# Optimization experiments

Measured on AMD Instinct MI355X. Metric: run time of the kernel, lower is better.

Reference implementation:

```python
import jax, jax.numpy as jnp
import numpy as np

B, C, H, W = 4, 192, 56, 56


def setup_inputs() -> dict:
    key = jax.random.key(0)
    k1, k2, k3 = jax.random.split(key, 3)
    x = jax.random.normal(k1, (B, C, H, W), dtype=jnp.float32)
    conv_w = jax.random.normal(k2, (C, 2 * C), dtype=jnp.float32) * (1.0 / np.sqrt(2 * C))
    conv_b = jax.random.normal(k3, (C,), dtype=jnp.float32) * 0.01
    bn_gamma = jnp.ones((C,), dtype=jnp.float32)
    bn_beta = jnp.zeros((C,), dtype=jnp.float32)
    bn_mean = jnp.zeros((C,), dtype=jnp.float32)
    bn_var = jnp.ones((C,), dtype=jnp.float32)
    return {"x": x, "conv_w": conv_w, "conv_b": conv_b, "bn_gamma": bn_gamma,
            "bn_beta": bn_beta, "bn_mean": bn_mean, "bn_var": bn_var, "K": 4}


def reference(x, conv_w, conv_b, bn_gamma, bn_beta, bn_mean, bn_var, K):
    b, c, h, w = x.shape
    shifts_h = list(range(0, h, K))          # rolls along H
    shifts_w = list(range(K, w, K))          # rolls along W
    n = len(shifts_h) + len(shifts_w)
    scale = n ** (-0.5)
    # (B, n, C, H, W): all circularly shifted copies (static shift set)
    rolled = jnp.stack([jnp.roll(x, i, axis=2) for i in shifts_h] +
                       [jnp.roll(x, j, axis=3) for j in shifts_w], axis=1)
    # scores: tanh(scale * x * x_rolled), summed over channels -> (B, n, 1, H, W)
    scores = jnp.tanh(rolled * x[:, None] * scale).sum(axis=2, keepdims=True)
    weights = jax.nn.softmax(scores, axis=1)
    out = (rolled * weights).sum(axis=1)     # (B, C, H, W)
    cat = jnp.concatenate([x, out], axis=1)  # (B, 2C, H, W)
    # 1x1 conv as GEMM over channels
    y = jnp.einsum('bchw,oc->bohw', cat, conv_w) + conv_b[None, :, None, None]
    # BatchNorm2d in eval mode (running stats)
    eps = 1e-5
    inv = bn_gamma / jnp.sqrt(bn_var + eps)
    y = (y - bn_mean[None, :, None, None]) * inv[None, :, None, None] + bn_beta[None, :, None, None]
    return jax.nn.gelu(y, approximate=False)
```

## Files before the change

kernel.cpp:

```cpp
#include <hip/hip_runtime.h>
#include <hip/hip_bf16.h>
#include <math.h>

#define BB 4
#define CC 192
#define HH 56
#define WW 56
#define HWW 3136

typedef __attribute__((ext_vector_type(8))) short short8;
typedef __attribute__((ext_vector_type(4))) float f32x4;

__device__ __forceinline__ unsigned short f2b(float f) {
    __hip_bfloat16 h = __float2bfloat16(f);
    return __builtin_bit_cast(unsigned short, h);
}
__device__ __forceinline__ float b2f(unsigned short u) {
    unsigned int x = ((unsigned int)u) << 16;
    return __builtin_bit_cast(float, x);
}
__device__ __forceinline__ void fma4(float4& a, float w, const float4& x) {
    a.x += w * x.x; a.y += w * x.y; a.z += w * x.z; a.w += w * x.w;
}

__global__ __launch_bounds__(256) void k_pre(const float* __restrict__ x,
                                             float* __restrict__ xt,
                                             const float* __restrict__ cw,
                                             unsigned short* __restrict__ cwh,
                                             unsigned short* __restrict__ cwl) {
    int tid = threadIdx.x;
    if (blockIdx.x < 2352) {
        __shared__ float tile[32][33];
        int id = blockIdx.x;
        int b = id / 588, rem = id % 588;
        int by = rem / 98, bx = rem % 98;
        int tx = tid & 31, ty = tid >> 5;
        int p0 = bx * 32, c0 = by * 32;
#pragma unroll
        for (int i = 0; i < 4; i++) {
            int c = c0 + ty + 8 * i;
            tile[ty + 8 * i][tx] = x[(b * CC + c) * HWW + p0 + tx];
        }
        __syncthreads();
#pragma unroll
        for (int i = 0; i < 4; i++) {
            int p = p0 + ty + 8 * i;
            xt[(size_t)(b * HWW + p) * CC + c0 + tx] = tile[tx][ty + 8 * i];
        }
    } else {
        int i = (blockIdx.x - 2352) * 256 + tid;
        if (i < CC * 576) {
            int o = i / 576, k = i % 576;
            int ks = (k >= 384) ? (k - 192) : k;
            float v = cw[o * 384 + ks];
            unsigned short hi = f2b(v);
            cwh[i] = hi;
            cwl[i] = f2b(v - b2f(hi));
        }
    }
}

__global__ __launch_bounds__(256) void k_scores(const float* __restrict__ xt,
                                                float* __restrict__ sp) {
    __shared__ float Xs[28 * 100];
    int bid = blockIdx.x, tid = threadIdx.x;
    bool isH = bid < 896;
    int lid = isH ? bid : bid - 896;
    int half = lid & 1;
    int rp = (lid >> 1) & 1;
    int cb = lid >> 2;
    int b = cb / 56, l0 = cb % 56;
    int r0 = rp * 2;

    const float* src = xt + (size_t)(b * HWW) * CC + half * 96;
    for (int idx = tid; idx < 28 * 24; idx += 256) {
        int t2 = idx / 24, cq = idx % 24;
        int pi = (r0 + t2 / 14) + 4 * (t2 % 14);
        int pix = isH ? (pi * WW + l0) : (l0 * WW + pi);
        float4 v = *(const float4*)(src + (size_t)pix * CC + cq * 4);
        *(float4*)&Xs[t2 * 100 + cq * 4] = v;
    }
    __syncthreads();

    const float K2 = 0.38490017945975050f;
    int perCls = isH ? 105 : 91;
    int nI = 2 * perCls;
    if (tid < nI) {
        int cls = tid / perCls, p = tid % perCls;
        int a, bb;
        if (isH) {
            a = (int)((sqrtf((float)(8 * p + 1)) - 1.0f) * 0.5f);
            bb = p - (a * (a + 1)) / 2;
        } else {
            int ap = (int)((sqrtf((float)(8 * p + 1)) - 1.0f) * 0.5f);
            bb = p - (ap * (ap + 1)) / 2;
            a = ap + 1;
        }
        const float* pA = &Xs[(cls * 14 + a) * 100];
        const float* pB = &Xs[(cls * 14 + bb) * 100];
        float s0 = 0.f, s1 = 0.f, s2 = 0.f, s3 = 0.f;
#pragma unroll
        for (int q = 0; q < 24; q++) {
            float4 av = *(const float4*)(pA + q * 4);
            float4 bv = *(const float4*)(pB + q * 4);
            s0 += __builtin_amdgcn_rcpf(__expf(av.x * bv.x * K2) + 1.0f);
            s1 += __builtin_amdgcn_rcpf(__expf(av.y * bv.y * K2) + 1.0f);
            s2 += __builtin_amdgcn_rcpf(__expf(av.z * bv.z * K2) + 1.0f);
            s3 += __builtin_amdgcn_rcpf(__expf(av.w * bv.w * K2) + 1.0f);
        }
        float s = 96.0f - 2.0f * (s0 + s1 + s2 + s3);
        int r = r0 + cls;
        size_t base = (size_t)(half * BB + b) * HWW;
        if (isH) {
            int i1 = a - bb;
            int h1 = r + 4 * a, h2 = r + 4 * bb;
            sp[(base + h1 * WW + l0) * 32 + i1] = s;
            if (a != bb) sp[(base + h2 * WW + l0) * 32 + (14 - i1)] = s;
        } else {
            int d = a - bb;
            int w1 = r + 4 * a, w2 = r + 4 * bb;
            sp[(base + l0 * WW + w1) * 32 + 14 + (d - 1)] = s;
            sp[(base + l0 * WW + w2) * 32 + 14 + (13 - d)] = s;
        }
    }
}

__global__ __launch_bounds__(192) void k_acc(const float* __restrict__ xt,
                                             const float* __restrict__ sp,
                                             unsigned short* __restrict__ oHh,
                                             unsigned short* __restrict__ oHl,
                                             unsigned short* __restrict__ oWh,
                                             unsigned short* __restrict__ oWl) {
    __shared__ float Wt[14 * 56];
    int bid = blockIdx.x, tid = threadIdx.x;
    bool isH = bid < 224;
    int lid = isH ? bid : bid - 224;
    int b = lid / 56, l0 = lid % 56;

    if (tid < 56) {
        int pix = isH ? (tid * WW + l0) : (l0 * WW + tid);
        const float4* p0 = (const float4*)&sp[((size_t)(0 * BB + b) * HWW + pix) * 32];
        const float4* p1 = (const float4*)&sp[((size_t)(1 * BB + b) * HWW + pix) * 32];
        float sc[28];
#pragma unroll
        for (int j = 0; j < 7; j++) {
            float4 u = p0[j], v = p1[j];
            sc[4 * j + 0] = u.x + v.x; sc[4 * j + 1] = u.y + v.y;
            sc[4 * j + 2] = u.z + v.z; sc[4 * j + 3] = u.w + v.w;
        }
        float mx = -1e30f;
#pragma unroll
        for (int s = 0; s < 27; s++) mx = fmaxf(mx, sc[s]);
        float sum = 0.f;
#pragma unroll
        for (int s = 0; s < 27; s++) { sc[s] = __expf(sc[s] - mx); sum += sc[s]; }
        float inv = __builtin_amdgcn_rcpf(sum);
        if (isH) {
#pragma unroll
            for (int i = 0; i < 14; i++) Wt[i * 56 + tid] = sc[i] * inv;
        } else {
#pragma unroll
            for (int j = 0; j < 13; j++) Wt[j * 56 + tid] = sc[14 + j] * inv;
        }
    }
    __syncthreads();
    {
        int r = tid & 3, q = tid >> 2;
        float4 in[14];
#pragma unroll
        for (int t = 0; t < 14; t++) {
            int pix = isH ? ((r + 4 * t) * WW + l0) : (l0 * WW + (r + 4 * t));
            in[t] = *(const float4*)(xt + (size_t)(b * HWW + pix) * CC + q * 4);
        }
        float4 acc[14] = {};
        if (isH) {
#pragma unroll
            for (int i = 0; i < 14; i++)
#pragma unroll
                for (int a = 0; a < 14; a++)
                    fma4(acc[a], Wt[i * 56 + (r + 4 * a)], in[(a - i + 14) % 14]);
        } else {
#pragma unroll
            for (int j = 0; j < 13; j++)
#pragma unroll
                for (int a = 0; a < 14; a++)
                    fma4(acc[a], Wt[j * 56 + (r + 4 * a)], in[(a - j - 1 + 14) % 14]);
        }
        unsigned short* dh = isH ? oHh : oWh;
        unsigned short* dl = isH ? oHl : oWl;
#pragma unroll
        for (int a = 0; a < 14; a++) {
            int pix = isH ? ((r + 4 * a) * WW + l0) : (l0 * WW + (r + 4 * a));
            size_t o = (size_t)(b * HWW + pix) * CC + q * 4;
            ushort4 hi4, lo4;
            hi4.x = f2b(acc[a].x); lo4.x = f2b(acc[a].x - b2f(hi4.x));
            hi4.y = f2b(acc[a].y); lo4.y = f2b(acc[a].y - b2f(hi4.y));
            hi4.z = f2b(acc[a].z); lo4.z = f2b(acc[a].z - b2f(hi4.z));
            hi4.w = f2b(acc[a].w); lo4.w = f2b(acc[a].w - b2f(hi4.w));
            *(ushort4*)(dh + o) = hi4;
            *(ushort4*)(dl + o) = lo4;
        }
    }
}

__global__ __launch_bounds__(256) void k_conv(const float* __restrict__ xt,
                                              const unsigned short* __restrict__ oHh,
                                              const unsigned short* __restrict__ oHl,
                                              const unsigned short* __restrict__ oWh,
                                              const unsigned short* __restrict__ oWl,
                                              const unsigned short* __restrict__ cwh,
                                              const unsigned short* __restrict__ cwl,
                                              const float* __restrict__ cb,
                                              const float* __restrict__ gma,
                                              const float* __restrict__ bta,
                                              const float* __restrict__ mea,
                                              const float* __restrict__ var,
                                              float* __restrict__ y) {
    __shared__ unsigned short AB[4 * 64 * 72];
    unsigned short* Ah = AB;
    unsigned short* Al = AB + 64 * 72;
    unsigned short* Bh = AB + 2 * 64 * 72;
    unsigned short* Bl = AB + 3 * 64 * 72;
    int bm = blockIdx.x * 64, bn = blockIdx.y * 64;
    int tid = threadIdx.x, lane = tid & 63, wv = tid >> 6;

    f32x4 acc[4] = {{0,0,0,0},{0,0,0,0},{0,0,0,0},{0,0,0,0}};

    for (int kc9 = 0; kc9 < 9; kc9++) {
#pragma unroll
        for (int r2 = 0; r2 < 2; r2++) {
            int idx = tid + r2 * 256;
            int m = idx >> 3, kq = idx & 7;
            if (kc9 < 3) {
                const float* s = xt + (size_t)(bm + m) * CC + kc9 * 64 + kq * 8;
                float4 v0 = *(const float4*)s;
                float4 v1 = *(const float4*)(s + 4);
                float v[8] = {v0.x, v0.y, v0.z, v0.w, v1.x, v1.y, v1.z, v1.w};
                unsigned short hi[8], lo[8];
#pragma unroll
                for (int e = 0; e < 8; e++) {
                    hi[e] = f2b(v[e]);
                    lo[e] = f2b(v[e] - b2f(hi[e]));
                }
                *(short8*)&Ah[m * 72 + kq * 8] = *(short8*)hi;
                *(short8*)&Al[m * 72 + kq * 8] = *(short8*)lo;
            } else {
                const unsigned short* sh;
                const unsigned short* sl;
                int coff;
                if (kc9 < 6) { sh = oHh; sl = oHl; coff = (kc9 - 3) * 64; }
                else         { sh = oWh; sl = oWl; coff = (kc9 - 6) * 64; }
                size_t ao = (size_t)(bm + m) * CC + coff + kq * 8;
                *(short8*)&Ah[m * 72 + kq * 8] = *(const short8*)(sh + ao);
                *(short8*)&Al[m * 72 + kq * 8] = *(const short8*)(sl + ao);
            }
            size_t bo = (size_t)(bn + m) * 576 + kc9 * 64 + kq * 8;
            *(short8*)&Bh[m * 72 + kq * 8] = *(const short8*)(cwh + bo);
            *(short8*)&Bl[m * 72 + kq * 8] = *(const short8*)(cwl + bo);
        }
        __syncthreads();
        int n0 = wv * 16;
        int k8 = lane >> 4;
        int col = lane & 15;
#pragma unroll
        for (int ks = 0; ks < 64; ks += 32) {
            int koff = ks + k8 * 8;
            short8 bfh = *(const short8*)&Bh[(n0 + col) * 72 + koff];
            short8 bfl = *(const short8*)&Bl[(n0 + col) * 72 + koff];
#pragma unroll
            for (int fm = 0; fm < 4; fm++) {
                short8 afh = *(const short8*)&Ah[(fm * 16 + col) * 72 + koff];
                short8 afl = *(const short8*)&Al[(fm * 16 + col) * 72 + koff];
                acc[fm] = __builtin_amdgcn_mfma_f32_16x16x32_bf16(afh, bfh, acc[fm], 0, 0, 0);
                acc[fm] = __builtin_amdgcn_mfma_f32_16x16x32_bf16(afl, bfh, acc[fm], 0, 0, 0);
                acc[fm] = __builtin_amdgcn_mfma_f32_16x16x32_bf16(afh, bfl, acc[fm], 0, 0, 0);
            }
        }
        __syncthreads();
    }

    float* Ds = (float*)AB;
    {
        int col = lane & 15, rowq = lane >> 4;
#pragma unroll
        for (int fm = 0; fm < 4; fm++)
#pragma unroll
            for (int rg = 0; rg < 4; rg++)
                Ds[(fm * 16 + rowq * 4 + rg) * 68 + wv * 16 + col] = acc[fm][rg];
    }
    __syncthreads();
    {
        int o = tid >> 2, mq0 = tid & 3;
        int oo = bn + o;
        float bias = cb[oo];
        float inv  = gma[oo] * rsqrtf(var[oo] + 1e-5f);
        float mean = mea[oo], beta = bta[oo];
        int b = bm / HWW, p0 = bm % HWW;
#pragma unroll
        for (int g = 0; g < 4; g++) {
            int mq = mq0 + g * 4;
            float v[4];
#pragma unroll
            for (int j = 0; j < 4; j++) {
                float t = Ds[(mq * 4 + j) * 68 + o] + bias;
                t = (t - mean) * inv + beta;
                v[j] = 0.5f * t * (1.0f + erff(t * 0.70710678118654752f));
            }
            float4 st; st.x = v[0]; st.y = v[1]; st.z = v[2]; st.w = v[3];
            *(float4*)&y[(size_t)(b * CC + oo) * HWW + p0 + mq * 4] = st;
        }
    }
}

extern "C" void kernel_launch(void* const* d_in, const int* in_sizes, int n_in,
                              void* d_out, int out_size, void* d_ws, size_t ws_size,
                              hipStream_t stream) {
    const float* x   = (const float*)d_in[0];
    const float* cw  = (const float*)d_in[1];
    const float* cb  = (const float*)d_in[2];
    const float* gma = (const float*)d_in[3];
    const float* bta = (const float*)d_in[4];
    const float* mea = (const float*)d_in[5];
    const float* var = (const float*)d_in[6];
    float* out = (float*)d_out;

    float* ws = (float*)d_ws;
    float*          xt  = ws;
    float*          sp  = ws + 2408448;
    unsigned short* oHh = (unsigned short*)(ws + 3211264);
    unsigned short* oHl = (unsigned short*)(ws + 4415488);
    unsigned short* oWh = (unsigned short*)(ws + 5619712);
    unsigned short* oWl = (unsigned short*)(ws + 6823936);
    unsigned short* cwh = (unsigned short*)(ws + 8028160);
    unsigned short* cwl = (unsigned short*)(ws + 8083456);

    k_pre<<<2784, 256, 0, stream>>>(x, xt, cw, cwh, cwl);
    k_scores<<<1792, 256, 0, stream>>>(xt, sp);
    k_acc<<<448, 192, 0, stream>>>(xt, sp, oHh, oHl, oWh, oWl);
    k_conv<<<dim3(196, 3), 256, 0, stream>>>(xt, oHh, oHl, oWh, oWl,
                                             cwh, cwl, cb, gma, bta, mea, var, out);
}
```

Measured before the change: 132.2 us.

## Apply 1x1 conv before shift-weighted accumulation and fuse epilogue into W pass

Uses linearity of the 1x1 conv to compute W·x once (N=384, K=192) before the softmax-weighted shifted sums, so the accumulation operates on projected features instead of feeding a K=576 GEMM. The scores computation and GEMM share one launch, and BN+GELU are fused into the W-direction accumulation kernel with an LDS transpose for NCHW output. It trades bf16 split intermediates for fp32 u/z/yp buffers and leaves the accumulation kernels with only 224 blocks each.

```diff
diff --git a/kernel.cpp b/kernel.cpp
--- a/kernel.cpp
+++ b/kernel.cpp
@@ -24,15 +24,14 @@
 }
 
 __global__ __launch_bounds__(256) void k_pre(const float* __restrict__ x,
+                                             const float* __restrict__ cw,
                                              float* __restrict__ xt,
-                                             const float* __restrict__ cw,
                                              unsigned short* __restrict__ cwh,
                                              unsigned short* __restrict__ cwl) {
-    int tid = threadIdx.x;
-    if (blockIdx.x < 2352) {
+    int tid = threadIdx.x, bid = blockIdx.x;
+    if (bid < 2352) {
         __shared__ float tile[32][33];
-        int id = blockIdx.x;
-        int b = id / 588, rem = id % 588;
+        int b = bid / 588, rem = bid % 588;
         int by = rem / 98, bx = rem % 98;
         int tx = tid & 31, ty = tid >> 5;
         int p0 = bx * 32, c0 = by * 32;
@@ -48,11 +47,10 @@
             xt[(size_t)(b * HWW + p) * CC + c0 + tx] = tile[tx][ty + 8 * i];
         }
     } else {
-        int i = (blockIdx.x - 2352) * 256 + tid;
-        if (i < CC * 576) {
-            int o = i / 576, k = i % 576;
-            int ks = (k >= 384) ? (k - 192) : k;
-            float v = cw[o * 384 + ks];
+        int i = (bid - 2352) * 256 + tid;
+        if (i < 384 * 192) {
+            int n = i / 192, k = i % 192;
+            float v = (n < 192) ? cw[n * 384 + k] : cw[(n - 192) * 384 + 192 + k];
             unsigned short hi = f2b(v);
             cwh[i] = hi;
             cwl[i] = f2b(v - b2f(hi));
@@ -60,93 +58,173 @@
     }
 }
 
-__global__ __launch_bounds__(256) void k_scores(const float* __restrict__ xt,
-                                                float* __restrict__ sp) {
-    __shared__ float Xs[28 * 100];
-    int bid = blockIdx.x, tid = threadIdx.x;
-    bool isH = bid < 896;
-    int lid = isH ? bid : bid - 896;
-    int half = lid & 1;
-    int rp = (lid >> 1) & 1;
-    int cb = lid >> 2;
-    int b = cb / 56, l0 = cb % 56;
-    int r0 = rp * 2;
-
-    const float* src = xt + (size_t)(b * HWW) * CC + half * 96;
-    for (int idx = tid; idx < 28 * 24; idx += 256) {
-        int t2 = idx / 24, cq = idx % 24;
-        int pi = (r0 + t2 / 14) + 4 * (t2 % 14);
-        int pix = isH ? (pi * WW + l0) : (l0 * WW + pi);
-        float4 v = *(const float4*)(src + (size_t)pix * CC + cq * 4);
-        *(float4*)&Xs[t2 * 100 + cq * 4] = v;
-    }
-    __syncthreads();
-
-    const float K2 = 0.38490017945975050f;
-    int perCls = isH ? 105 : 91;
-    int nI = 2 * perCls;
-    if (tid < nI) {
-        int cls = tid / perCls, p = tid % perCls;
-        int a, bb;
-        if (isH) {
-            a = (int)((sqrtf((float)(8 * p + 1)) - 1.0f) * 0.5f);
-            bb = p - (a * (a + 1)) / 2;
-        } else {
-            int ap = (int)((sqrtf((float)(8 * p + 1)) - 1.0f) * 0.5f);
-            bb = p - (ap * (ap + 1)) / 2;
-            a = ap + 1;
-        }
-        const float* pA = &Xs[(cls * 14 + a) * 100];
-        const float* pB = &Xs[(cls * 14 + bb) * 100];
-        float s0 = 0.f, s1 = 0.f, s2 = 0.f, s3 = 0.f;
-#pragma unroll
-        for (int q = 0; q < 24; q++) {
-            float4 av = *(const float4*)(pA + q * 4);
-            float4 bv = *(const float4*)(pB + q * 4);
-            s0 += __builtin_amdgcn_rcpf(__expf(av.x * bv.x * K2) + 1.0f);
-            s1 += __builtin_amdgcn_rcpf(__expf(av.y * bv.y * K2) + 1.0f);
-            s2 += __builtin_amdgcn_rcpf(__expf(av.z * bv.z * K2) + 1.0f);
-            s3 += __builtin_amdgcn_rcpf(__expf(av.w * bv.w * K2) + 1.0f);
-        }
-        float s = 96.0f - 2.0f * (s0 + s1 + s2 + s3);
-        int r = r0 + cls;
-        size_t base = (size_t)(half * BB + b) * HWW;
-        if (isH) {
-            int i1 = a - bb;
-            int h1 = r + 4 * a, h2 = r + 4 * bb;
-            sp[(base + h1 * WW + l0) * 32 + i1] = s;
-            if (a != bb) sp[(base + h2 * WW + l0) * 32 + (14 - i1)] = s;
-        } else {
-            int d = a - bb;
-            int w1 = r + 4 * a, w2 = r + 4 * bb;
-            sp[(base + l0 * WW + w1) * 32 + 14 + (d - 1)] = s;
-            sp[(base + l0 * WW + w2) * 32 + 14 + (13 - d)] = s;
-        }
-    }
-}
-
-__global__ __launch_bounds__(192) void k_acc(const float* __restrict__ xt,
-                                             const float* __restrict__ sp,
-                                             unsigned short* __restrict__ oHh,
-                                             unsigned short* __restrict__ oHl,
-                                             unsigned short* __restrict__ oWh,
-                                             unsigned short* __restrict__ oWl) {
+__global__ __launch_bounds__(256) void k_mid(const float* __restrict__ xt,
+                                             const unsigned short* __restrict__ cwh,
+                                             const unsigned short* __restrict__ cwl,
+                                             float* __restrict__ sp,
+                                             float* __restrict__ u,
+                                             float* __restrict__ z) {
+    __shared__ __align__(16) char smem[36864];
+    int tid = threadIdx.x, bid = blockIdx.x;
+
+    if (bid < 1792) {
+        float* Xs = (float*)smem;
+        const float K2 = 0.38490017945975050f;
+        bool isH = bid < 896;
+        int lid = isH ? bid : bid - 896;
+        int half = lid & 1;
+        int rp = (lid >> 1) & 1;
+        int cb2 = lid >> 2;
+        int b = cb2 / 56, l0 = cb2 % 56;
+        int r0 = rp * 2;
+
+        const float* src = xt + (size_t)(b * HWW) * CC + half * 96;
+        for (int idx = tid; idx < 28 * 24; idx += 256) {
+            int t2 = idx / 24, cq = idx % 24;
+            int pi = (r0 + t2 / 14) + 4 * (t2 % 14);
+            int pix = isH ? (pi * WW + l0) : (l0 * WW + pi);
+            float4 v = *(const float4*)(src + (size_t)pix * CC + cq * 4);
+            *(float4*)&Xs[t2 * 100 + cq * 4] = v;
+        }
+        __syncthreads();
+
+        int perCls = isH ? 105 : 91;
+        if (tid < 2 * perCls) {
+            int cls = tid / perCls, p = tid % perCls;
+            int a, bb;
+            if (isH) {
+                a = (int)((sqrtf((float)(8 * p + 1)) - 1.0f) * 0.5f);
+                bb = p - (a * (a + 1)) / 2;
+            } else {
+                int ap = (int)((sqrtf((float)(8 * p + 1)) - 1.0f) * 0.5f);
+                bb = p - (ap * (ap + 1)) / 2;
+                a = ap + 1;
+            }
+            const float* pA = &Xs[(cls * 14 + a) * 100];
+            const float* pB = &Xs[(cls * 14 + bb) * 100];
+            float s0 = 0.f, s1 = 0.f, s2 = 0.f, s3 = 0.f;
+#pragma unroll
+            for (int q = 0; q < 24; q++) {
+                float4 av = *(const float4*)(pA + q * 4);
+                float4 bv = *(const float4*)(pB + q * 4);
+                s0 += __builtin_amdgcn_rcpf(__expf(av.x * bv.x * K2) + 1.0f);
+                s1 += __builtin_amdgcn_rcpf(__expf(av.y * bv.y * K2) + 1.0f);
+                s2 += __builtin_amdgcn_rcpf(__expf(av.z * bv.z * K2) + 1.0f);
+                s3 += __builtin_amdgcn_rcpf(__expf(av.w * bv.w * K2) + 1.0f);
+            }
+            float s = 96.0f - 2.0f * (s0 + s1 + s2 + s3);
+            int r = r0 + cls;
+            size_t base = (size_t)(half * BB + b) * HWW;
+            if (isH) {
+                int i1 = a - bb;
+                int h1 = r + 4 * a, h2 = r + 4 * bb;
+                sp[(base + h1 * WW + l0) * 32 + i1] = s;
+                if (a != bb) sp[(base + h2 * WW + l0) * 32 + (14 - i1)] = s;
+            } else {
+                int d = a - bb;
+                int w1 = r + 4 * a, w2 = r + 4 * bb;
+                sp[(base + l0 * WW + w1) * 32 + 14 + (d - 1)] = s;
+                sp[(base + l0 * WW + w2) * 32 + 14 + (13 - d)] = s;
+            }
+        }
+        return;
+    }
+
+    {
+        unsigned short* Ah = (unsigned short*)smem;
+        unsigned short* Al = Ah + 64 * 72;
+        unsigned short* Bh = Ah + 2 * 64 * 72;
+        unsigned short* Bl = Ah + 3 * 64 * 72;
+        float* Ds = (float*)smem;
+        int vb = bid - 1792;
+        int bm = (vb % 196) * 64, bn = (vb / 196) * 64;
+        int lane = tid & 63, wv = tid >> 6;
+
+        f32x4 acc[4] = {{0,0,0,0},{0,0,0,0},{0,0,0,0},{0,0,0,0}};
+
+        for (int kc = 0; kc < 3; kc++) {
+#pragma unroll
+            for (int r2 = 0; r2 < 2; r2++) {
+                int idx = tid + r2 * 256;
+                int m = idx >> 3, kq = idx & 7;
+                const float* s = xt + (size_t)(bm + m) * CC + kc * 64 + kq * 8;
+                float4 v0 = *(const float4*)s;
+                float4 v1 = *(const float4*)(s + 4);
+                float vv[8] = {v0.x, v0.y, v0.z, v0.w, v1.x, v1.y, v1.z, v1.w};
+                unsigned short hi[8], lo[8];
+#pragma unroll
+                for (int e = 0; e < 8; e++) {
+                    hi[e] = f2b(vv[e]);
+                    lo[e] = f2b(vv[e] - b2f(hi[e]));
+                }
+                *(short8*)&Ah[m * 72 + kq * 8] = *(short8*)hi;
+                *(short8*)&Al[m * 72 + kq * 8] = *(short8*)lo;
+                size_t bo = (size_t)(bn + m) * 192 + kc * 64 + kq * 8;
+                *(short8*)&Bh[m * 72 + kq * 8] = *(const short8*)(cwh + bo);
+                *(short8*)&Bl[m * 72 + kq * 8] = *(const short8*)(cwl + bo);
+            }
+            __syncthreads();
+            int n0 = wv * 16;
+            int k8 = lane >> 4;
+            int col = lane & 15;
+#pragma unroll
+            for (int ks = 0; ks < 64; ks += 32) {
+                int koff = ks + k8 * 8;
+                short8 bfh = *(const short8*)&Bh[(n0 + col) * 72 + koff];
+                short8 bfl = *(const short8*)&Bl[(n0 + col) * 72 + koff];
+#pragma unroll
+                for (int fm = 0; fm < 4; fm++) {
+                    short8 afh = *(const short8*)&Ah[(fm * 16 + col) * 72 + koff];
+                    short8 afl = *(const short8*)&Al[(fm * 16 + col) * 72 + koff];
+                    acc[fm] = __builtin_amdgcn_mfma_f32_16x16x32_bf16(afh, bfh, acc[fm], 0, 0, 0);
+                    acc[fm] = __builtin_amdgcn_mfma_f32_16x16x32_bf16(afl, bfh, acc[fm], 0, 0, 0);
+                    acc[fm] = __builtin_amdgcn_mfma_f32_16x16x32_bf16(afh, bfl, acc[fm], 0, 0, 0);
+                }
+            }
+            __syncthreads();
+        }
+        {
+            int col = lane & 15, rowq = lane >> 4;
+#pragma unroll
+            for (int fm = 0; fm < 4; fm++)
+#pragma unroll
+                for (int rg = 0; rg < 4; rg++)
+                    Ds[(fm * 16 + rowq * 4 + rg) * 68 + wv * 16 + col] = acc[fm][rg];
+        }
+        __syncthreads();
+        {
+            int c4 = tid & 15, m0 = tid >> 4;
+            int cg = bn + c4 * 4;
+            float* dst = (cg < 192) ? u : z;
+            int cc = (cg < 192) ? cg : cg - 192;
+#pragma unroll
+            for (int p = 0; p < 4; p++) {
+                int m = m0 + p * 16;
+                float4 v = *(float4*)&Ds[m * 68 + c4 * 4];
+                *(float4*)&dst[(size_t)(bm + m) * CC + cc] = v;
+            }
+        }
+    }
+}
+
+__global__ __launch_bounds__(192) void k_accH(const float* __restrict__ u,
+                                              const float* __restrict__ z,
+                                              const float* __restrict__ sp,
+                                              float* __restrict__ yp) {
     __shared__ float Wt[14 * 56];
     int bid = blockIdx.x, tid = threadIdx.x;
-    bool isH = bid < 224;
-    int lid = isH ? bid : bid - 224;
-    int b = lid / 56, l0 = lid % 56;
+    int b = bid / 56, l0 = bid % 56;
 
     if (tid < 56) {
-        int pix = isH ? (tid * WW + l0) : (l0 * WW + tid);
+        int pix = tid * WW + l0;
         const float4* p0 = (const float4*)&sp[((size_t)(0 * BB + b) * HWW + pix) * 32];
         const float4* p1 = (const float4*)&sp[((size_t)(1 * BB + b) * HWW + pix) * 32];
         float sc[28];
 #pragma unroll
         for (int j = 0; j < 7; j++) {
-            float4 u = p0[j], v = p1[j];
-            sc[4 * j + 0] = u.x + v.x; sc[4 * j + 1] = u.y + v.y;
-            sc[4 * j + 2] = u.z + v.z; sc[4 * j + 3] = u.w + v.w;
+            float4 a = p0[j], v = p1[j];
+            sc[4 * j + 0] = a.x + v.x; sc[4 * j + 1] = a.y + v.y;
+            sc[4 * j + 2] = a.z + v.z; sc[4 * j + 3] = a.w + v.w;
         }
         float mx = -1e30f;
 #pragma unroll
@@ -155,13 +233,8 @@
 #pragma unroll
         for (int s = 0; s < 27; s++) { sc[s] = __expf(sc[s] - mx); sum += sc[s]; }
         float inv = __builtin_amdgcn_rcpf(sum);
-        if (isH) {
-#pragma unroll
-            for (int i = 0; i < 14; i++) Wt[i * 56 + tid] = sc[i] * inv;
-        } else {
-#pragma unroll
-            for (int j = 0; j < 13; j++) Wt[j * 56 + tid] = sc[14 + j] * inv;
-        }
+#pragma unroll
+        for (int i = 0; i < 14; i++) Wt[i * 56 + tid] = sc[i] * inv;
     }
     __syncthreads();
     {
@@ -169,145 +242,119 @@
         float4 in[14];
 #pragma unroll
         for (int t = 0; t < 14; t++) {
-            int pix = isH ? ((r + 4 * t) * WW + l0) : (l0 * WW + (r + 4 * t));
-            in[t] = *(const float4*)(xt + (size_t)(b * HWW + pix) * CC + q * 4);
-        }
-        float4 acc[14] = {};
-        if (isH) {
-#pragma unroll
-            for (int i = 0; i < 14; i++)
-#pragma unroll
-                for (int a = 0; a < 14; a++)
-                    fma4(acc[a], Wt[i * 56 + (r + 4 * a)], in[(a - i + 14) % 14]);
-        } else {
-#pragma unroll
-            for (int j = 0; j < 13; j++)
-#pragma unroll
-                for (int a = 0; a < 14; a++)
-                    fma4(acc[a], Wt[j * 56 + (r + 4 * a)], in[(a - j - 1 + 14) % 14]);
-        }
-        unsigned short* dh = isH ? oHh : oWh;
-        unsigned short* dl = isH ? oHl : oWl;
+            int pix = (r + 4 * t) * WW + l0;
+            in[t] = *(const float4*)(z + (size_t)(b * HWW + pix) * CC + q * 4);
+        }
+        float4 acc[14];
 #pragma unroll
         for (int a = 0; a < 14; a++) {
-            int pix = isH ? ((r + 4 * a) * WW + l0) : (l0 * WW + (r + 4 * a));
-            size_t o = (size_t)(b * HWW + pix) * CC + q * 4;
-            ushort4 hi4, lo4;
-            hi4.x = f2b(acc[a].x); lo4.x = f2b(acc[a].x - b2f(hi4.x));
-            hi4.y = f2b(acc[a].y); lo4.y = f2b(acc[a].y - b2f(hi4.y));
-            hi4.z = f2b(acc[a].z); lo4.z = f2b(acc[a].z - b2f(hi4.z));
-            hi4.w = f2b(acc[a].w); lo4.w = f2b(acc[a].w - b2f(hi4.w));
-            *(ushort4*)(dh + o) = hi4;
-            *(ushort4*)(dl + o) = lo4;
-        }
-    }
-}
-
-__global__ __launch_bounds__(256) void k_conv(const float* __restrict__ xt,
-                                              const unsigned short* __restrict__ oHh,
-                                              const unsigned short* __restrict__ oHl,
-                                              const unsigned short* __restrict__ oWh,
-                                              const unsigned short* __restrict__ oWl,
-                                              const unsigned short* __restrict__ cwh,
-                                              const unsigned short* __restrict__ cwl,
+            int pix = (r + 4 * a) * WW + l0;
+            acc[a] = *(const float4*)(u + (size_t)(b * HWW + pix) * CC + q * 4);
+        }
+#pragma unroll
+        for (int i = 0; i < 14; i++)
+#pragma unroll
+            for (int a = 0; a < 14; a++)
+                fma4(acc[a], Wt[i * 56 + (r + 4 * a)], in[(a - i + 14) % 14]);
+#pragma unroll
+        for (int a = 0; a < 14; a++) {
+            int pix = (r + 4 * a) * WW + l0;
+            *(float4*)(yp + (size_t)(b * HWW + pix) * CC + q * 4) = acc[a];
+        }
+    }
+}
+
+__global__ __launch_bounds__(192) void k_accW(const float* __restrict__ yp,
+                                              const float* __restrict__ z,
+                                              const float* __restrict__ sp,
                                               const float* __restrict__ cb,
                                               const float* __restrict__ gma,
                                               const float* __restrict__ bta,
                                               const float* __restrict__ mea,
                                               const float* __restrict__ var,
                                               float* __restrict__ y) {
-    __shared__ unsigned short AB[4 * 64 * 72];
-    unsigned short* Ah = AB;
-    unsigned short* Al = AB + 64 * 72;
-    unsigned short* Bh = AB + 2 * 64 * 72;
-    unsigned short* Bl = AB + 3 * 64 * 72;
-    int bm = blockIdx.x * 64, bn = blockIdx.y * 64;
-    int tid = threadIdx.x, lane = tid & 63, wv = tid >> 6;
-
-    f32x4 acc[4] = {{0,0,0,0},{0,0,0,0},{0,0,0,0},{0,0,0,0}};
-
-    for (int kc9 = 0; kc9 < 9; kc9++) {
-#pragma unroll
-        for (int r2 = 0; r2 < 2; r2++) {
-            int idx = tid + r2 * 256;
-            int m = idx >> 3, kq = idx & 7;
-            if (kc9 < 3) {
-                const float* s = xt + (size_t)(bm + m) * CC + kc9 * 64 + kq * 8;
-                float4 v0 = *(const float4*)s;
-                float4 v1 = *(const float4*)(s + 4);
-                float v[8] = {v0.x, v0.y, v0.z, v0.w, v1.x, v1.y, v1.z, v1.w};
-                unsigned short hi[8], lo[8];
-#pragma unroll
-                for (int e = 0; e < 8; e++) {
-                    hi[e] = f2b(v[e]);
-                    lo[e] = f2b(v[e] - b2f(hi[e]));
-                }
-                *(short8*)&Ah[m * 72 + kq * 8] = *(short8*)hi;
-                *(short8*)&Al[m * 72 + kq * 8] = *(short8*)lo;
-            } else {
-                const unsigned short* sh;
-                const unsigned short* sl;
-                int coff;
-                if (kc9 < 6) { sh = oHh; sl = oHl; coff = (kc9 - 3) * 64; }
-                else         { sh = oWh; sl = oWl; coff = (kc9 - 6) * 64; }
-                size_t ao = (size_t)(bm + m) * CC + coff + kq * 8;
-                *(short8*)&Ah[m * 72 + kq * 8] = *(const short8*)(sh + ao);
-                *(short8*)&Al[m * 72 + kq * 8] = *(const short8*)(sl + ao);
-            }
-            size_t bo = (size_t)(bn + m) * 576 + kc9 * 64 + kq * 8;
-            *(short8*)&Bh[m * 72 + kq * 8] = *(const short8*)(cwh + bo);
-            *(short8*)&Bl[m * 72 + kq * 8] = *(const short8*)(cwl + bo);
-        }
-        __syncthreads();
-        int n0 = wv * 16;
-        int k8 = lane >> 4;
-        int col = lane & 15;
-#pragma unroll
-        for (int ks = 0; ks < 64; ks += 32) {
-            int koff = ks + k8 * 8;
-            short8 bfh = *(const short8*)&Bh[(n0 + col) * 72 + koff];
-            short8 bfl = *(const short8*)&Bl[(n0 + col) * 72 + koff];
-#pragma unroll
-            for (int fm = 0; fm < 4; fm++) {
-                short8 afh = *(const short8*)&Ah[(fm * 16 + col) * 72 + koff];
-                short8 afl = *(const short8*)&Al[(fm * 16 + col) * 72 + koff];
-                acc[fm] = __builtin_amdgcn_mfma_f32_16x16x32_bf16(afh, bfh, acc[fm], 0, 0, 0);
-                acc[fm] = __builtin_amdgcn_mfma_f32_16x16x32_bf16(afl, bfh, acc[fm], 0, 0, 0);
-                acc[fm] = __builtin_amdgcn_mfma_f32_16x16x32_bf16(afh, bfl, acc[fm], 0, 0, 0);
-            }
-        }
-        __syncthreads();
-    }
-
-    float* Ds = (float*)AB;
-    {
-        int col = lane & 15, rowq = lane >> 4;
-#pragma unroll
-        for (int fm = 0; fm < 4; fm++)
-#pragma unroll
-            for (int rg = 0; rg < 4; rg++)
-                Ds[(fm * 16 + rowq * 4 + rg) * 68 + wv * 16 + col] = acc[fm][rg];
+    __shared__ float Wt[14 * 56];
+    __shared__ float Ys[56 * 196];
+    int bid = blockIdx.x, tid = threadIdx.x;
+    int b = bid / 56, l0 = bid % 56;
+
+    if (tid < 56) {
+        int pix = l0 * WW + tid;
+        const float4* p0 = (const float4*)&sp[((size_t)(0 * BB + b) * HWW + pix) * 32];
+        const float4* p1 = (const float4*)&sp[((size_t)(1 * BB + b) * HWW + pix) * 32];
+        float sc[28];
+#pragma unroll
+        for (int j = 0; j < 7; j++) {
+            float4 a = p0[j], v = p1[j];
+            sc[4 * j + 0] = a.x + v.x; sc[4 * j + 1] = a.y + v.y;
+            sc[4 * j + 2] = a.z + v.z; sc[4 * j + 3] = a.w + v.w;
+        }
+        float mx = -1e30f;
+#pragma unroll
+        for (int s = 0; s < 27; s++) mx = fmaxf(mx, sc[s]);
+        float sum = 0.f;
+#pragma unroll
+        for (int s = 0; s < 27; s++) { sc[s] = __expf(sc[s] - mx); sum += sc[s]; }
+        float inv = __builtin_amdgcn_rcpf(sum);
+#pragma unroll
+        for (int j = 0; j < 13; j++) Wt[j * 56 + tid] = sc[14 + j] * inv;
     }
     __syncthreads();
     {
-        int o = tid >> 2, mq0 = tid & 3;
-        int oo = bn + o;
-        float bias = cb[oo];
-        float inv  = gma[oo] * rsqrtf(var[oo] + 1e-5f);
-        float mean = mea[oo], beta = bta[oo];
-        int b = bm / HWW, p0 = bm % HWW;
-#pragma unroll
-        for (int g = 0; g < 4; g++) {
-            int mq = mq0 + g * 4;
-            float v[4];
-#pragma unroll
-            for (int j = 0; j < 4; j++) {
-                float t = Ds[(mq * 4 + j) * 68 + o] + bias;
-                t = (t - mean) * inv + beta;
-                v[j] = 0.5f * t * (1.0f + erff(t * 0.70710678118654752f));
-            }
-            float4 st; st.x = v[0]; st.y = v[1]; st.z = v[2]; st.w = v[3];
-            *(float4*)&y[(size_t)(b * CC + oo) * HWW + p0 + mq * 4] = st;
+        int r = tid & 3, q = tid >> 2;
+        float4 in[14];
+#pragma unroll
+        for (int t = 0; t < 14; t++) {
+            int pix = l0 * WW + (r + 4 * t);
+            in[t] = *(const float4*)(z + (size_t)(b * HWW + pix) * CC + q * 4);
+        }
+        float4 acc[14];
+#pragma unroll
+        for (int a = 0; a < 14; a++) {
+            int pix = l0 * WW + (r + 4 * a);
+            acc[a] = *(const float4*)(yp + (size_t)(b * HWW + pix) * CC + q * 4);
+        }
+#pragma unroll
+        for (int j = 0; j < 13; j++)
+#pragma unroll
+            for (int a = 0; a < 14; a++)
+                fma4(acc[a], Wt[j * 56 + (r + 4 * a)], in[(a - j - 1 + 14) % 14]);
+
+        float4 bias4 = *(const float4*)&cb[q * 4];
+        float4 g4 = *(const float4*)&gma[q * 4];
+        float4 bt4 = *(const float4*)&bta[q * 4];
+        float4 me4 = *(const float4*)&mea[q * 4];
+        float4 va4 = *(const float4*)&var[q * 4];
+        float inv0 = g4.x * rsqrtf(va4.x + 1e-5f);
+        float inv1 = g4.y * rsqrtf(va4.y + 1e-5f);
+        float inv2 = g4.z * rsqrtf(va4.z + 1e-5f);
+        float inv3 = g4.w * rsqrtf(va4.w + 1e-5f);
+#pragma unroll
+        for (int a = 0; a < 14; a++) {
+            int w = r + 4 * a;
+            float4 t = acc[a];
+            t.x = (t.x + bias4.x - me4.x) * inv0 + bt4.x;
+            t.y = (t.y + bias4.y - me4.y) * inv1 + bt4.y;
+            t.z = (t.z + bias4.z - me4.z) * inv2 + bt4.z;
+            t.w = (t.w + bias4.w - me4.w) * inv3 + bt4.w;
+            t.x = 0.5f * t.x * (1.0f + erff(t.x * 0.70710678118654752f));
+            t.y = 0.5f * t.y * (1.0f + erff(t.y * 0.70710678118654752f));
+            t.z = 0.5f * t.z * (1.0f + erff(t.z * 0.70710678118654752f));
+            t.w = 0.5f * t.w * (1.0f + erff(t.w * 0.70710678118654752f));
+            *(float4*)&Ys[w * 196 + q * 4] = t;
+        }
+    }
+    __syncthreads();
+    {
+        int c = tid;
+#pragma unroll
+        for (int w4 = 0; w4 < 14; w4++) {
+            float4 v;
+            v.x = Ys[(w4 * 4 + 0) * 196 + c];
+            v.y = Ys[(w4 * 4 + 1) * 196 + c];
+            v.z = Ys[(w4 * 4 + 2) * 196 + c];
+            v.w = Ys[(w4 * 4 + 3) * 196 + c];
+            *(float4*)&y[(size_t)(b * CC + c) * HWW + l0 * WW + w4 * 4] = v;
         }
     }
 }
@@ -327,16 +374,14 @@
     float* ws = (float*)d_ws;
     float*          xt  = ws;
     float*          sp  = ws + 2408448;
-    unsigned short* oHh = (unsigned short*)(ws + 3211264);
-    unsigned short* oHl = (unsigned short*)(ws + 4415488);
-    unsigned short* oWh = (unsigned short*)(ws + 5619712);
-    unsigned short* oWl = (unsigned short*)(ws + 6823936);
-    unsigned short* cwh = (unsigned short*)(ws + 8028160);
-    unsigned short* cwl = (unsigned short*)(ws + 8083456);
-
-    k_pre<<<2784, 256, 0, stream>>>(x, xt, cw, cwh, cwl);
-    k_scores<<<1792, 256, 0, stream>>>(xt, sp);
-    k_acc<<<448, 192, 0, stream>>>(xt, sp, oHh, oHl, oWh, oWl);
-    k_conv<<<dim3(196, 3), 256, 0, stream>>>(xt, oHh, oHl, oWh, oWl,
-                                             cwh, cwl, cb, gma, bta, mea, var, out);
-}
+    float*          u   = ws + 3211264;
+    float*          z   = ws + 5619712;
+    float*          yp  = ws + 8028160;
+    unsigned short* cwh = (unsigned short*)(ws + 10436608);
+    unsigned short* cwl = (unsigned short*)(ws + 10473472);
+
+    k_pre<<<2640, 256, 0, stream>>>(x, cw, xt, cwh, cwl);
+    k_mid<<<2968, 256, 0, stream>>>(xt, cwh, cwl, sp, u, z);
+    k_accH<<<224, 192, 0, stream>>>(u, z, sp, yp);
+    k_accW<<<224, 192, 0, stream>>>(yp, z, sp, cb, gma, bta, mea, var, out);
+}
```

Result: faster. 127.9 us (-3.2%).
